# Optimization experiments

Hardware: AMD Instinct MI355X
Metric: run time of the kernel (lower is better)

The kernel has to match this reference:

```python
import jax, jax.numpy as jnp
import numpy as np

N_ENTITIES = 100000
N_EDGES = 500000
N_RELATIONS = 200
DIM = 64
HEADS = 4
POW_ITER = 5
ALPHA = 0.1
LEAKY_SLOPE = 0.01
EPS = 1e-16


def setup_inputs() -> dict:
    key = jax.random.key(0)
    ks = jax.random.split(key, 11)
    scale = 0.1
    return {
        "entity_embed": jax.random.normal(ks[0], (N_ENTITIES, DIM), jnp.float32),
        "relation_embed": jax.random.normal(ks[1], (N_RELATIONS, DIM), jnp.float32),
        "W_h": jax.random.normal(ks[2], (DIM, HEADS * DIM), jnp.float32) * scale,
        "W_t": jax.random.normal(ks[3], (DIM, HEADS * DIM), jnp.float32) * scale,
        "W_r": jax.random.normal(ks[4], (DIM, HEADS * DIM), jnp.float32) * scale,
        "att_h": jax.random.normal(ks[5], (HEADS, DIM), jnp.float32) * scale,
        "att_t": jax.random.normal(ks[6], (HEADS, DIM), jnp.float32) * scale,
        "att_r": jax.random.normal(ks[7], (HEADS, DIM), jnp.float32) * scale,
        "W_o": jax.random.normal(ks[8], (HEADS * DIM, DIM), jnp.float32) * scale,
        "edge_index": jax.random.randint(ks[9], (2, N_EDGES), 0, N_ENTITIES, jnp.int64),
        "edge_type": jax.random.randint(ks[10], (N_EDGES,), 0, N_RELATIONS, jnp.int64),
    }


def _segment_softmax(scores, seg_ids, num_segments):
    # scores: [E, heads]; softmax over edges sharing the same seg_id, per head
    m = jax.ops.segment_max(scores, seg_ids, num_segments=num_segments)
    e = jnp.exp(scores - m[seg_ids])
    denom = jax.ops.segment_sum(e, seg_ids, num_segments=num_segments)
    return e / (denom[seg_ids] + EPS)


def reference(entity_embed, relation_embed, W_h, W_t, W_r,
              att_h, att_t, att_r, W_o, edge_index, edge_type):
    head_ids, tail_ids = edge_index[0], edge_index[1]

    # per-edge gathered embeddings, projected per head: [E, heads, dim]
    Wh = (entity_embed[head_ids] @ W_h).reshape(-1, HEADS, DIM)
    Wt = (entity_embed[tail_ids] @ W_t).reshape(-1, HEADS, DIM)
    Wr = (relation_embed[edge_type] @ W_r).reshape(-1, HEADS, DIM)

    s_h = jnp.sum(jnp.tanh(Wh) * att_h[None], axis=-1)  # [E, heads]
    s_t = jnp.sum(jnp.tanh(Wt) * att_t[None], axis=-1)
    s_r = jnp.sum(jnp.tanh(Wr) * att_r[None], axis=-1)
    scores = jax.nn.leaky_relu(s_h + s_t + s_r, negative_slope=LEAKY_SLOPE)

    att = _segment_softmax(scores, head_ids, N_ENTITIES)  # [E, heads]
    A = (1.0 - ALPHA) * att

    # PPR power iteration, vectorized over heads: Z: [N, heads, dim]
    Z0 = entity_embed[:, None, :]  # [N, 1, dim]
    Z_init = jnp.broadcast_to(Z0, (N_ENTITIES, HEADS, DIM))

    def step(Z, _):
        msgs = A[:, :, None] * Z[tail_ids]  # [E, heads, dim]
        Z_new = jax.ops.segment_sum(msgs, head_ids, num_segments=N_ENTITIES) + ALPHA * Z0
        return Z_new, None

    Z, _ = jax.lax.scan(step, Z_init, None, length=POW_ITER)

    out = Z.reshape(N_ENTITIES, HEADS * DIM) @ W_o  # [N, dim]
    return out
```

## Files before the change

kernel.cpp:

```cpp
#include <hip/hip_runtime.h>
#include <hip/hip_fp16.h>
#include <math.h>

#define N_ENT 100000
#define N_EDGE 500000
#define N_REL 200

typedef short bf16x8 __attribute__((ext_vector_type(8)));
typedef float f32x4 __attribute__((ext_vector_type(4)));

__device__ __forceinline__ float fast_tanh(float x) {
    float xc = fminf(x, 15.f);
    float e = __expf(2.f * xc);
    return (e - 1.f) / (e + 1.f);
}

__device__ __forceinline__ unsigned short f2bf(float f) {
    unsigned u = __float_as_uint(f);
    unsigned r = u + 0x7FFF + ((u >> 16) & 1);
    return (unsigned short)(r >> 16);
}

__device__ __forceinline__ uint2 pack_half4(const float4 v) {
    __half2 lo = __floats2half2_rn(v.x, v.y);
    __half2 hi = __floats2half2_rn(v.z, v.w);
    uint2 r;
    r.x = *reinterpret_cast<const unsigned int*>(&lo);
    r.y = *reinterpret_cast<const unsigned int*>(&hi);
    return r;
}

__device__ __forceinline__ float4 unpack_half4(uint2 u) {
    __half2 lo = *reinterpret_cast<const __half2*>(&u.x);
    __half2 hi = *reinterpret_cast<const __half2*>(&u.y);
    float2 a = __half22float2(lo);
    float2 b = __half22float2(hi);
    return make_float4(a.x, a.y, b.x, b.y);
}

__global__ __launch_bounds__(256) void cvt_emb_kernel(
    const float* __restrict__ in, unsigned short* __restrict__ out, int nquads)
{
    for (int i = blockIdx.x * 256 + threadIdx.x; i < nquads; i += gridDim.x * 256) {
        float4 v = ((const float4*)in)[i];
        ushort4 o;
        o.x = f2bf(v.x); o.y = f2bf(v.y); o.z = f2bf(v.z); o.w = f2bf(v.w);
        ((ushort4*)out)[i] = o;
    }
}

__global__ __launch_bounds__(256) void cvt_wT_kernel(
    const float* __restrict__ W0, const float* __restrict__ W1,
    unsigned short* __restrict__ wT)
{
    int idx = blockIdx.x * 256 + threadIdx.x;
    if (idx >= 2 * 256 * 64) return;
    int mat = idx >> 14;
    int rem = idx & 16383;
    int col = rem >> 6;
    int k   = rem & 63;
    const float* W = (mat == 0) ? W0 : W1;
    wT[idx] = f2bf(W[k * 256 + col]);
}

__global__ __launch_bounds__(256) void proj_mfma_kernel(
    const unsigned short* __restrict__ emb_bf,
    const unsigned short* __restrict__ wT,
    const float* __restrict__ att0, const float* __restrict__ att1,
    float* __restrict__ p0, float* __restrict__ p1, int nrows)
{
    const int wv   = threadIdx.x >> 6;
    const int lane = threadIdx.x & 63;
    const int r4   = lane >> 4;
    const int cl   = lane & 15;
    const int rowbase = blockIdx.x * 64 + wv * 16;

    int ra = min(rowbase + cl, nrows - 1);
    bf16x8 a0 = *(const bf16x8*)(emb_bf + (size_t)ra * 64 + 8 * r4);
    bf16x8 a1 = *(const bf16x8*)(emb_bf + (size_t)ra * 64 + 8 * r4 + 32);

#pragma unroll
    for (int mat = 0; mat < 2; ++mat) {
        const float* att = (mat == 0) ? att0 : att1;
        float* p         = (mat == 0) ? p0 : p1;
        float pacc[4][4];
#pragma unroll
        for (int head = 0; head < 4; ++head) {
            float ph_[4] = {0.f, 0.f, 0.f, 0.f};
#pragma unroll
            for (int sub = 0; sub < 4; ++sub) {
                int col = head * 64 + sub * 16 + cl;
                const unsigned short* wp =
                    wT + ((size_t)(mat * 256 + col)) * 64 + 8 * r4;
                bf16x8 b0 = *(const bf16x8*)(wp);
                bf16x8 b1 = *(const bf16x8*)(wp + 32);
                f32x4 c = {0.f, 0.f, 0.f, 0.f};
                c = __builtin_amdgcn_mfma_f32_16x16x32_bf16(a0, b0, c, 0, 0, 0);
                c = __builtin_amdgcn_mfma_f32_16x16x32_bf16(a1, b1, c, 0, 0, 0);
                float av = att[head * 64 + sub * 16 + cl];
#pragma unroll
                for (int j = 0; j < 4; ++j) {
                    float v = fast_tanh(c[j]) * av;
                    v += __shfl_xor(v, 1, 64);
                    v += __shfl_xor(v, 2, 64);
                    v += __shfl_xor(v, 4, 64);
                    v += __shfl_xor(v, 8, 64);
                    ph_[j] += v;
                }
            }
#pragma unroll
            for (int j = 0; j < 4; ++j) pacc[head][j] = ph_[j];
        }
        if (cl == 0) {
#pragma unroll
            for (int j = 0; j < 4; ++j) {
                int row = rowbase + r4 * 4 + j;
                if (row < nrows) {
                    *(float4*)(p + (size_t)row * 4) = make_float4(
                        pacc[0][j], pacc[1][j], pacc[2][j], pacc[3][j]);
                }
            }
        }
    }
}

__global__ __launch_bounds__(256) void proj_gemm_kernel(
    const float* __restrict__ emb,
    const float* __restrict__ W0,
    const float* __restrict__ att0,
    float* __restrict__ p0,
    int nrows)
{
    __shared__ float e_lds[64][68];
    __shared__ float w0_lds[64][64];
    __shared__ float red[4][4][64];

    const int t    = threadIdx.x;
    const int wv   = t >> 6;
    const int lane = t & 63;
    const int er   = t & 15;
    const int d0   = (t >> 4) * 4;
    const int base = blockIdx.x * 64;

#pragma unroll
    for (int i = 0; i < 4; ++i) {
        int f = t + 256 * i;
        int row = f >> 4, c4 = f & 15;
        int gr = min(base + row, nrows - 1);
        float4 v = *(const float4*)(emb + (size_t)gr * 64 + 4 * c4);
        *(float4*)&e_lds[row][4 * c4] = v;
    }

    float p0s[4][4];

    for (int head = 0; head < 4; ++head) {
        {
            int k0 = t >> 4, c4 = t & 15;
#pragma unroll
            for (int kk = 0; kk < 4; ++kk) {
                int k = k0 + 16 * kk;
                *(float4*)&w0_lds[k][4 * c4] =
                    *(const float4*)(W0 + (size_t)k * 256 + head * 64 + 4 * c4);
            }
        }
        __syncthreads();

        float acc0[4][4] = {};
        for (int k4 = 0; k4 < 16; ++k4) {
            float4 z0 = *(const float4*)&e_lds[er +  0][4 * k4];
            float4 z1 = *(const float4*)&e_lds[er + 16][4 * k4];
            float4 z2 = *(const float4*)&e_lds[er + 32][4 * k4];
            float4 z3 = *(const float4*)&e_lds[er + 48][4 * k4];
            const float zr[4][4] = {
                {z0.x, z0.y, z0.z, z0.w},
                {z1.x, z1.y, z1.z, z1.w},
                {z2.x, z2.y, z2.z, z2.w},
                {z3.x, z3.y, z3.z, z3.w}};
#pragma unroll
            for (int jj = 0; jj < 4; ++jj) {
                float4 w0v = *(const float4*)&w0_lds[4 * k4 + jj][d0];
#pragma unroll
                for (int i = 0; i < 4; ++i) {
                    float zj = zr[i][jj];
                    acc0[i][0] = fmaf(zj, w0v.x, acc0[i][0]);
                    acc0[i][1] = fmaf(zj, w0v.y, acc0[i][1]);
                    acc0[i][2] = fmaf(zj, w0v.z, acc0[i][2]);
                    acc0[i][3] = fmaf(zj, w0v.w, acc0[i][3]);
                }
            }
        }

        float4 av0 = *(const float4*)(att0 + head * 64 + d0);
#pragma unroll
        for (int i = 0; i < 4; ++i) {
            float v = fast_tanh(acc0[i][0]) * av0.x
                    + fast_tanh(acc0[i][1]) * av0.y
                    + fast_tanh(acc0[i][2]) * av0.z
                    + fast_tanh(acc0[i][3]) * av0.w;
            v += __shfl_xor(v, 16, 64);
            v += __shfl_xor(v, 32, 64);
            p0s[head][i] = v;
        }
        __syncthreads();
    }

    if (lane < 16) {
#pragma unroll
        for (int h = 0; h < 4; ++h)
#pragma unroll
            for (int i = 0; i < 4; ++i)
                red[wv][h][lane + 16 * i] = p0s[h][i];
    }
    __syncthreads();
    if (t < 64) {
        int row = base + t;
        if (row < nrows) {
            float4 pv;
            pv.x = red[0][0][t] + red[1][0][t] + red[2][0][t] + red[3][0][t];
            pv.y = red[0][1][t] + red[1][1][t] + red[2][1][t] + red[3][1][t];
            pv.z = red[0][2][t] + red[1][2][t] + red[2][2][t] + red[3][2][t];
            pv.w = red[0][3][t] + red[1][3][t] + red[2][3][t] + red[3][3][t];
            *(float4*)(p0 + (size_t)row * 4) = pv;
        }
    }
}

__global__ __launch_bounds__(256) void hist_kernel(
    const int* __restrict__ eidx, int* __restrict__ counts)
{
    int e = blockIdx.x * 256 + threadIdx.x;
    if (e >= N_EDGE) return;
    atomicAdd(&counts[eidx[e]], 1);
}

__global__ __launch_bounds__(1024) void scan_kernel(
    const int* __restrict__ counts, int* __restrict__ row_start)
{
    __shared__ int wsum[16];
    __shared__ int carry_s;
    const int lane = threadIdx.x & 63;
    const int wid  = threadIdx.x >> 6;
    if (threadIdx.x == 0) carry_s = 0;
    __syncthreads();
    for (int base = 0; base < N_ENT; base += 4096) {
        int i0 = base + (int)threadIdx.x * 4;
        int4 v = make_int4(0, 0, 0, 0);
        if (i0 + 3 < N_ENT) v = *(const int4*)(counts + i0);
        else {
            if (i0 + 0 < N_ENT) v.x = counts[i0 + 0];
            if (i0 + 1 < N_ENT) v.y = counts[i0 + 1];
            if (i0 + 2 < N_ENT) v.z = counts[i0 + 2];
            if (i0 + 3 < N_ENT) v.w = counts[i0 + 3];
        }
        int s1 = v.x + v.y, s2 = s1 + v.z, tsum = s2 + v.w;
        int incl = tsum;
#pragma unroll
        for (int off = 1; off < 64; off <<= 1) {
            int t = __shfl_up(incl, off, 64);
            if (lane >= off) incl += t;
        }
        if (lane == 63) wsum[wid] = incl;
        __syncthreads();
        int wave_off = 0;
#pragma unroll
        for (int w = 0; w < 16; ++w)
            wave_off += (w < wid) ? wsum[w] : 0;
        int carry = carry_s;
        int excl = carry + wave_off + (incl - tsum);
        if (i0 + 3 < N_ENT) {
            *(int4*)(row_start + i0) = make_int4(excl, excl + v.x, excl + s1, excl + s2);
        } else {
            if (i0 + 0 < N_ENT) row_start[i0 + 0] = excl;
            if (i0 + 1 < N_ENT) row_start[i0 + 1] = excl + v.x;
            if (i0 + 2 < N_ENT) row_start[i0 + 2] = excl + s1;
            if (i0 + 3 < N_ENT) row_start[i0 + 3] = excl + s2;
        }
        __syncthreads();
        if (threadIdx.x == 1023) carry_s = carry + wave_off + incl;
    }
    __syncthreads();
    if (threadIdx.x == 0) row_start[N_ENT] = carry_s;
}

__global__ __launch_bounds__(256) void scatter_score_kernel(
    const int* __restrict__ eidx, const int* __restrict__ etype,
    const float* __restrict__ ph, const float* __restrict__ pt,
    const float* __restrict__ pr,
    const int* __restrict__ row_start, int* __restrict__ cursor,
    int* __restrict__ csr_col, float* __restrict__ csr_a)
{
    int e = blockIdx.x * 256 + threadIdx.x;
    if (e >= N_EDGE) return;
    int hn = eidx[e];
    int tn = eidx[N_EDGE + e];
    int r  = etype[e];
    float4 a = *(const float4*)(ph + (size_t)hn * 4);
    float4 b = *(const float4*)(pt + (size_t)tn * 4);
    float4 c = *(const float4*)(pr + (size_t)r * 4);
    float s0 = a.x + b.x + c.x;
    float s1 = a.y + b.y + c.y;
    float s2 = a.z + b.z + c.z;
    float s3 = a.w + b.w + c.w;
    s0 = s0 >= 0.f ? s0 : 0.01f * s0;
    s1 = s1 >= 0.f ? s1 : 0.01f * s1;
    s2 = s2 >= 0.f ? s2 : 0.01f * s2;
    s3 = s3 >= 0.f ? s3 : 0.01f * s3;
    float4 ev = make_float4(__expf(s0), __expf(s1), __expf(s2), __expf(s3));
    int pos = row_start[hn] + atomicAdd(&cursor[hn], 1);
    csr_col[pos] = tn;
    *(float4*)(csr_a + (size_t)pos * 4) = ev;
}

__global__ __launch_bounds__(256) void normalize_kernel(
    const int* __restrict__ row_start, float* __restrict__ csr_a)
{
    const int wid  = threadIdx.x >> 6;
    const int lane = threadIdx.x & 63;
    const int n = blockIdx.x * 4 + wid;
    if (n >= N_ENT) return;
    const int s   = row_start[n];
    const int end = row_start[n + 1];
    const int nf  = (end - s) * 4;

    float sum = 0.f;
    for (int f = lane; f < nf; f += 64)
        sum += csr_a[(size_t)s * 4 + f];
#pragma unroll
    for (int off = 4; off < 64; off <<= 1)
        sum += __shfl_xor(sum, off, 64);
    float scale = 0.9f / (sum + 1e-16f);
    for (int f = lane; f < nf; f += 64)
        csr_a[(size_t)s * 4 + f] *= scale;
}

template <bool IN_HALF, bool OUT_HALF>
__global__ __launch_bounds__(256) void spmm_kernel(
    const void* __restrict__ Zin_v, const float* __restrict__ emb,
    const int* __restrict__ row_start, const int* __restrict__ csr_col,
    const float* __restrict__ csr_a, void* __restrict__ Zout_v)
{
    const int wave = threadIdx.x >> 6;
    const int lane = threadIdx.x & 63;
    const int n = blockIdx.x * 4 + wave;
    const int h = lane >> 4;
    const __half* Zin_h = (const __half*)Zin_v;

    const float4* e4 = (const float4*)emb;
    float4 zi = e4[(size_t)n * 16 + (lane & 15)];
    float4 acc0 = make_float4(0.1f * zi.x, 0.1f * zi.y, 0.1f * zi.z, 0.1f * zi.w);
    float4 acc1 = make_float4(0.f, 0.f, 0.f, 0.f);
    float4 acc2 = make_float4(0.f, 0.f, 0.f, 0.f);
    float4 acc3 = make_float4(0.f, 0.f, 0.f, 0.f);

    const int s   = row_start[n];
    const int end = row_start[n + 1];

    auto zrow = [&](int c) -> float4 {
        if (IN_HALF) {
            uint2 u = *(const uint2*)(Zin_h + (size_t)c * 256 + 4 * lane);
            return unpack_half4(u);
        } else {
            return *(const float4*)(emb + (size_t)c * 64 + 4 * (lane & 15));
        }
    };
    auto fma4 = [](float4& acc, float a, const float4& z) {
        acc.x = fmaf(a, z.x, acc.x);
        acc.y = fmaf(a, z.y, acc.y);
        acc.z = fmaf(a, z.z, acc.z);
        acc.w = fmaf(a, z.w, acc.w);
    };

    for (int b = s; b < end; b += 16) {
        const int nb = min(16, end - b);
        int   cl = (lane < nb) ? csr_col[b + lane] : 0;
        float al = (lane < nb * 4) ? csr_a[(size_t)b * 4 + lane] : 0.f;

        int j = 0;
        for (; j + 4 <= nb; j += 4) {
            int c0 = __shfl(cl, j + 0, 64);
            int c1 = __shfl(cl, j + 1, 64);
            int c2 = __shfl(cl, j + 2, 64);
            int c3 = __shfl(cl, j + 3, 64);
            float a0 = __shfl(al, (j + 0) * 4 + h, 64);
            float a1 = __shfl(al, (j + 1) * 4 + h, 64);
            float a2 = __shfl(al, (j + 2) * 4 + h, 64);
            float a3 = __shfl(al, (j + 3) * 4 + h, 64);
            float4 za = zrow(c0);
            float4 zb = zrow(c1);
            float4 zc = zrow(c2);
            float4 zd = zrow(c3);
            fma4(acc0, a0, za);
            fma4(acc1, a1, zb);
            fma4(acc2, a2, zc);
            fma4(acc3, a3, zd);
        }
        if (j + 0 < nb) {
            int c = __shfl(cl, j + 0, 64);
            float a = __shfl(al, (j + 0) * 4 + h, 64);
            float4 z = zrow(c);
            fma4(acc0, a, z);
        }
        if (j + 1 < nb) {
            int c = __shfl(cl, j + 1, 64);
            float a = __shfl(al, (j + 1) * 4 + h, 64);
            float4 z = zrow(c);
            fma4(acc1, a, z);
        }
        if (j + 2 < nb) {
            int c = __shfl(cl, j + 2, 64);
            float a = __shfl(al, (j + 2) * 4 + h, 64);
            float4 z = zrow(c);
            fma4(acc2, a, z);
        }
    }
    acc0.x += acc1.x + acc2.x + acc3.x;
    acc0.y += acc1.y + acc2.y + acc3.y;
    acc0.z += acc1.z + acc2.z + acc3.z;
    acc0.w += acc1.w + acc2.w + acc3.w;

    if (OUT_HALF)
        *(uint2*)((__half*)Zout_v + (size_t)n * 256 + 4 * lane) = pack_half4(acc0);
    else
        *(float4*)((float*)Zout_v + (size_t)n * 256 + 4 * lane) = acc0;
}

__global__ __launch_bounds__(256) void outproj_kernel(
    const float* __restrict__ Z, const float* __restrict__ Wo,
    float* __restrict__ out)
{
    __shared__ float z_lds[64][68];
    __shared__ float w_lds[64][64];
    const int t = threadIdx.x;
    const int base = blockIdx.x * 64;
    const int er = t & 15;
    const int d0 = (t >> 4) * 4;

    float acc[4][4] = {};
    for (int kc = 0; kc < 4; ++kc) {
        {
            const float4* src = (const float4*)(Wo + (size_t)kc * 64 * 64);
            float4* dst = (float4*)&w_lds[0][0];
#pragma unroll
            for (int i = 0; i < 4; ++i)
                dst[t + 256 * i] = src[t + 256 * i];
        }
        {
#pragma unroll
            for (int i = 0; i < 4; ++i) {
                int f = t + 256 * i;
                int row = f >> 4, c4 = f & 15;
                int gr = min(base + row, N_ENT - 1);
                float4 v = *(const float4*)(Z + (size_t)gr * 256 + kc * 64 + 4 * c4);
                *(float4*)&z_lds[row][4 * c4] = v;
            }
        }
        __syncthreads();

        for (int k4 = 0; k4 < 16; ++k4) {
            float4 z0 = *(const float4*)&z_lds[er +  0][4 * k4];
            float4 z1 = *(const float4*)&z_lds[er + 16][4 * k4];
            float4 z2 = *(const float4*)&z_lds[er + 32][4 * k4];
            float4 z3 = *(const float4*)&z_lds[er + 48][4 * k4];
#pragma unroll
            for (int jj = 0; jj < 4; ++jj) {
                float4 wv = *(const float4*)&w_lds[4 * k4 + jj][d0];
                float zj0 = ((const float*)&z0)[jj];
                float zj1 = ((const float*)&z1)[jj];
                float zj2 = ((const float*)&z2)[jj];
                float zj3 = ((const float*)&z3)[jj];
                acc[0][0] = fmaf(zj0, wv.x, acc[0][0]);
                acc[0][1] = fmaf(zj0, wv.y, acc[0][1]);
                acc[0][2] = fmaf(zj0, wv.z, acc[0][2]);
                acc[0][3] = fmaf(zj0, wv.w, acc[0][3]);
                acc[1][0] = fmaf(zj1, wv.x, acc[1][0]);
                acc[1][1] = fmaf(zj1, wv.y, acc[1][1]);
                acc[1][2] = fmaf(zj1, wv.z, acc[1][2]);
                acc[1][3] = fmaf(zj1, wv.w, acc[1][3]);
                acc[2][0] = fmaf(zj2, wv.x, acc[2][0]);
                acc[2][1] = fmaf(zj2, wv.y, acc[2][1]);
                acc[2][2] = fmaf(zj2, wv.z, acc[2][2]);
                acc[2][3] = fmaf(zj2, wv.w, acc[2][3]);
                acc[3][0] = fmaf(zj3, wv.x, acc[3][0]);
                acc[3][1] = fmaf(zj3, wv.y, acc[3][1]);
                acc[3][2] = fmaf(zj3, wv.z, acc[3][2]);
                acc[3][3] = fmaf(zj3, wv.w, acc[3][3]);
            }
        }
        __syncthreads();
    }

#pragma unroll
    for (int i = 0; i < 4; ++i) {
        int row = base + er + 16 * i;
        if (row < N_ENT) {
            *(float4*)(out + (size_t)row * 64 + d0) =
                make_float4(acc[i][0], acc[i][1], acc[i][2], acc[i][3]);
        }
    }
}

extern "C" void kernel_launch(void* const* d_in, const int* in_sizes, int n_in,
                              void* d_out, int out_size, void* d_ws, size_t ws_size,
                              hipStream_t stream)
{
    const float* entity = (const float*)d_in[0];
    const float* rel    = (const float*)d_in[1];
    const float* W_h    = (const float*)d_in[2];
    const float* W_t    = (const float*)d_in[3];
    const float* W_r    = (const float*)d_in[4];
    const float* att_h  = (const float*)d_in[5];
    const float* att_t  = (const float*)d_in[6];
    const float* att_r  = (const float*)d_in[7];
    const float* W_o    = (const float*)d_in[8];
    const int*   eidx   = (const int*)d_in[9];
    const int*   etype  = (const int*)d_in[10];
    float* out = (float*)d_out;

    char* ws = (char*)d_ws;
    size_t off = 0;
    auto alloc = [&](size_t bytes) -> void* {
        void* p = ws + off;
        off += (bytes + 255) & ~(size_t)255;
        return p;
    };
    float* p_h      = (float*)alloc((size_t)N_ENT * 4 * 4);
    float* p_t      = (float*)alloc((size_t)N_ENT * 4 * 4);
    float* p_r      = (float*)alloc((size_t)N_REL * 4 * 4);
    int*   counts   = (int*)alloc((size_t)N_ENT * 4);
    int*   row_start= (int*)alloc(((size_t)N_ENT + 1) * 4);
    int*   cursor   = (int*)alloc((size_t)N_ENT * 4);
    int*   csr_col  = (int*)alloc((size_t)N_EDGE * 4);
    float* csr_a    = (float*)alloc((size_t)N_EDGE * 4 * 4);
    float* Zf       = (float*)alloc((size_t)N_ENT * 256 * 4);
    __half* Zh_b    = (__half*)Zf;
    __half* Zh_a    = (__half*)alloc((size_t)N_ENT * 256 * 2);
    unsigned short* emb_bf = (unsigned short*)alloc((size_t)N_ENT * 64 * 2);
    unsigned short* wT     = (unsigned short*)alloc((size_t)2 * 256 * 64 * 2);

    hipMemsetAsync(counts, 0, (size_t)N_ENT * 4, stream);
    hipMemsetAsync(cursor, 0, (size_t)N_ENT * 4, stream);

    cvt_emb_kernel<<<2048, 256, 0, stream>>>(entity, emb_bf, N_ENT * 64 / 4);
    cvt_wT_kernel<<<(2 * 256 * 64 + 255) / 256, 256, 0, stream>>>(W_h, W_t, wT);

    proj_mfma_kernel<<<(N_ENT + 63) / 64, 256, 0, stream>>>(
        emb_bf, wT, att_h, att_t, p_h, p_t, N_ENT);
    proj_gemm_kernel<<<(N_REL + 63) / 64, 256, 0, stream>>>(
        rel, W_r, att_r, p_r, N_REL);

    hist_kernel<<<(N_EDGE + 255) / 256, 256, 0, stream>>>(eidx, counts);
    scan_kernel<<<1, 1024, 0, stream>>>(counts, row_start);
    scatter_score_kernel<<<(N_EDGE + 255) / 256, 256, 0, stream>>>(
        eidx, etype, p_h, p_t, p_r, row_start, cursor, csr_col, csr_a);
    normalize_kernel<<<(N_ENT + 3) / 4, 256, 0, stream>>>(row_start, csr_a);

    spmm_kernel<false, true ><<<N_ENT / 4, 256, 0, stream>>>(nullptr, entity, row_start, csr_col, csr_a, Zh_b);
    spmm_kernel<true,  true ><<<N_ENT / 4, 256, 0, stream>>>(Zh_b, entity, row_start, csr_col, csr_a, Zh_a);
    spmm_kernel<true,  true ><<<N_ENT / 4, 256, 0, stream>>>(Zh_a, entity, row_start, csr_col, csr_a, Zh_b);
    spmm_kernel<true,  true ><<<N_ENT / 4, 256, 0, stream>>>(Zh_b, entity, row_start, csr_col, csr_a, Zh_a);
    spmm_kernel<true,  false><<<N_ENT / 4, 256, 0, stream>>>(Zh_a, entity, row_start, csr_col, csr_a, Zf);

    outproj_kernel<<<(N_ENT + 63) / 64, 256, 0, stream>>>(Zf, W_o, out);
}
```

Before: 497.8 us.

## Use fp16 MFMA for output projection and keep final Z in half

The last power-iteration step now writes Z in fp16 instead of fp32. The output projection is replaced by an MFMA kernel that reads the fp16 Z directly and uses a transposed fp16 copy of W_o made by a new conversion kernel. This halves Z traffic on the final write and read, and moves the scalar-FMA LDS GEMM onto matrix cores. The projection kernel also defers its cross-lane shuffle reduction until after the sub-tile accumulation, cutting shuffles. The cost is extra rounding of the final Z and of W_o to fp16, plus one small extra launch.

```diff
diff --git a/kernel.cpp b/kernel.cpp
--- a/kernel.cpp
+++ b/kernel.cpp
@@ -7,6 +7,7 @@
 #define N_REL 200
 
 typedef short bf16x8 __attribute__((ext_vector_type(8)));
+typedef _Float16 f16x8 __attribute__((ext_vector_type(8)));
 typedef float f32x4 __attribute__((ext_vector_type(4)));
 
 __device__ __forceinline__ float fast_tanh(float x) {
@@ -63,6 +64,16 @@
     wT[idx] = f2bf(W[k * 256 + col]);
 }
 
+__global__ __launch_bounds__(256) void cvt_woT_kernel(
+    const float* __restrict__ Wo, __half* __restrict__ woT)
+{
+    int idx = blockIdx.x * 256 + threadIdx.x;
+    if (idx >= 64 * 256) return;
+    int d = idx >> 8;
+    int k = idx & 255;
+    woT[idx] = __float2half(Wo[k * 64 + d]);
+}
+
 __global__ __launch_bounds__(256) void proj_mfma_kernel(
     const unsigned short* __restrict__ emb_bf,
     const unsigned short* __restrict__ wT,
@@ -86,7 +97,7 @@
         float pacc[4][4];
 #pragma unroll
         for (int head = 0; head < 4; ++head) {
-            float ph_[4] = {0.f, 0.f, 0.f, 0.f};
+            float vsum[4] = {0.f, 0.f, 0.f, 0.f};
 #pragma unroll
             for (int sub = 0; sub < 4; ++sub) {
                 int col = head * 64 + sub * 16 + cl;
@@ -99,17 +110,18 @@
                 c = __builtin_amdgcn_mfma_f32_16x16x32_bf16(a1, b1, c, 0, 0, 0);
                 float av = att[head * 64 + sub * 16 + cl];
 #pragma unroll
-                for (int j = 0; j < 4; ++j) {
-                    float v = fast_tanh(c[j]) * av;
-                    v += __shfl_xor(v, 1, 64);
-                    v += __shfl_xor(v, 2, 64);
-                    v += __shfl_xor(v, 4, 64);
-                    v += __shfl_xor(v, 8, 64);
-                    ph_[j] += v;
-                }
+                for (int j = 0; j < 4; ++j)
+                    vsum[j] = fmaf(fast_tanh(c[j]), av, vsum[j]);
             }
 #pragma unroll
-            for (int j = 0; j < 4; ++j) pacc[head][j] = ph_[j];
+            for (int j = 0; j < 4; ++j) {
+                float v = vsum[j];
+                v += __shfl_xor(v, 1, 64);
+                v += __shfl_xor(v, 2, 64);
+                v += __shfl_xor(v, 4, 64);
+                v += __shfl_xor(v, 8, 64);
+                pacc[head][j] = v;
+            }
         }
         if (cl == 0) {
 #pragma unroll
@@ -424,77 +436,39 @@
         *(float4*)((float*)Zout_v + (size_t)n * 256 + 4 * lane) = acc0;
 }
 
-__global__ __launch_bounds__(256) void outproj_kernel(
-    const float* __restrict__ Z, const float* __restrict__ Wo,
+__global__ __launch_bounds__(256) void outproj_mfma_kernel(
+    const __half* __restrict__ Z,
+    const __half* __restrict__ woT,
     float* __restrict__ out)
 {
-    __shared__ float z_lds[64][68];
-    __shared__ float w_lds[64][64];
-    const int t = threadIdx.x;
-    const int base = blockIdx.x * 64;
-    const int er = t & 15;
-    const int d0 = (t >> 4) * 4;
-
-    float acc[4][4] = {};
-    for (int kc = 0; kc < 4; ++kc) {
-        {
-            const float4* src = (const float4*)(Wo + (size_t)kc * 64 * 64);
-            float4* dst = (float4*)&w_lds[0][0];
-#pragma unroll
-            for (int i = 0; i < 4; ++i)
-                dst[t + 256 * i] = src[t + 256 * i];
-        }
-        {
-#pragma unroll
-            for (int i = 0; i < 4; ++i) {
-                int f = t + 256 * i;
-                int row = f >> 4, c4 = f & 15;
-                int gr = min(base + row, N_ENT - 1);
-                float4 v = *(const float4*)(Z + (size_t)gr * 256 + kc * 64 + 4 * c4);
-                *(float4*)&z_lds[row][4 * c4] = v;
-            }
-        }
-        __syncthreads();
-
-        for (int k4 = 0; k4 < 16; ++k4) {
-            float4 z0 = *(const float4*)&z_lds[er +  0][4 * k4];
-            float4 z1 = *(const float4*)&z_lds[er + 16][4 * k4];
-            float4 z2 = *(const float4*)&z_lds[er + 32][4 * k4];
-            float4 z3 = *(const float4*)&z_lds[er + 48][4 * k4];
-#pragma unroll
-            for (int jj = 0; jj < 4; ++jj) {
-                float4 wv = *(const float4*)&w_lds[4 * k4 + jj][d0];
-                float zj0 = ((const float*)&z0)[jj];
-                float zj1 = ((const float*)&z1)[jj];
-                float zj2 = ((const float*)&z2)[jj];
-                float zj3 = ((const float*)&z3)[jj];
-                acc[0][0] = fmaf(zj0, wv.x, acc[0][0]);
-                acc[0][1] = fmaf(zj0, wv.y, acc[0][1]);
-                acc[0][2] = fmaf(zj0, wv.z, acc[0][2]);
-                acc[0][3] = fmaf(zj0, wv.w, acc[0][3]);
-                acc[1][0] = fmaf(zj1, wv.x, acc[1][0]);
-                acc[1][1] = fmaf(zj1, wv.y, acc[1][1]);
-                acc[1][2] = fmaf(zj1, wv.z, acc[1][2]);
-                acc[1][3] = fmaf(zj1, wv.w, acc[1][3]);
-                acc[2][0] = fmaf(zj2, wv.x, acc[2][0]);
-                acc[2][1] = fmaf(zj2, wv.y, acc[2][1]);
-                acc[2][2] = fmaf(zj2, wv.z, acc[2][2]);
-                acc[2][3] = fmaf(zj2, wv.w, acc[2][3]);
-                acc[3][0] = fmaf(zj3, wv.x, acc[3][0]);
-                acc[3][1] = fmaf(zj3, wv.y, acc[3][1]);
-                acc[3][2] = fmaf(zj3, wv.z, acc[3][2]);
-                acc[3][3] = fmaf(zj3, wv.w, acc[3][3]);
-            }
-        }
-        __syncthreads();
-    }
-
-#pragma unroll
-    for (int i = 0; i < 4; ++i) {
-        int row = base + er + 16 * i;
-        if (row < N_ENT) {
-            *(float4*)(out + (size_t)row * 64 + d0) =
-                make_float4(acc[i][0], acc[i][1], acc[i][2], acc[i][3]);
+    const int wv   = threadIdx.x >> 6;
+    const int lane = threadIdx.x & 63;
+    const int cl   = lane & 15;
+    const int r4   = lane >> 4;
+    const int rowbase = blockIdx.x * 64 + wv * 16;
+
+    int ra = min(rowbase + cl, N_ENT - 1);
+    const _Float16* zp = (const _Float16*)(Z + (size_t)ra * 256);
+    f16x8 a[8];
+#pragma unroll
+    for (int ks = 0; ks < 8; ++ks)
+        a[ks] = *(const f16x8*)(zp + ks * 32 + 8 * r4);
+
+    const _Float16* wp = (const _Float16*)woT;
+#pragma unroll
+    for (int st = 0; st < 4; ++st) {
+        f32x4 c = {0.f, 0.f, 0.f, 0.f};
+        const _Float16* wcol = wp + (size_t)(st * 16 + cl) * 256 + 8 * r4;
+#pragma unroll
+        for (int ks = 0; ks < 8; ++ks) {
+            f16x8 b = *(const f16x8*)(wcol + ks * 32);
+            c = __builtin_amdgcn_mfma_f32_16x16x32_f16(a[ks], b, c, 0, 0, 0);
+        }
+#pragma unroll
+        for (int j = 0; j < 4; ++j) {
+            int row = rowbase + r4 * 4 + j;
+            if (row < N_ENT)
+                out[(size_t)row * 64 + st * 16 + cl] = c[j];
         }
     }
 }
@@ -531,17 +505,18 @@
     int*   cursor   = (int*)alloc((size_t)N_ENT * 4);
     int*   csr_col  = (int*)alloc((size_t)N_EDGE * 4);
     float* csr_a    = (float*)alloc((size_t)N_EDGE * 4 * 4);
-    float* Zf       = (float*)alloc((size_t)N_ENT * 256 * 4);
-    __half* Zh_b    = (__half*)Zf;
     __half* Zh_a    = (__half*)alloc((size_t)N_ENT * 256 * 2);
+    __half* Zh_b    = (__half*)alloc((size_t)N_ENT * 256 * 2);
     unsigned short* emb_bf = (unsigned short*)alloc((size_t)N_ENT * 64 * 2);
     unsigned short* wT     = (unsigned short*)alloc((size_t)2 * 256 * 64 * 2);
+    __half* woT     = (__half*)alloc((size_t)64 * 256 * 2);
 
     hipMemsetAsync(counts, 0, (size_t)N_ENT * 4, stream);
     hipMemsetAsync(cursor, 0, (size_t)N_ENT * 4, stream);
 
     cvt_emb_kernel<<<2048, 256, 0, stream>>>(entity, emb_bf, N_ENT * 64 / 4);
     cvt_wT_kernel<<<(2 * 256 * 64 + 255) / 256, 256, 0, stream>>>(W_h, W_t, wT);
+    cvt_woT_kernel<<<(64 * 256 + 255) / 256, 256, 0, stream>>>(W_o, woT);
 
     proj_mfma_kernel<<<(N_ENT + 63) / 64, 256, 0, stream>>>(
         emb_bf, wT, att_h, att_t, p_h, p_t, N_ENT);
@@ -558,7 +533,7 @@
     spmm_kernel<true,  true ><<<N_ENT / 4, 256, 0, stream>>>(Zh_b, entity, row_start, csr_col, csr_a, Zh_a);
     spmm_kernel<true,  true ><<<N_ENT / 4, 256, 0, stream>>>(Zh_a, entity, row_start, csr_col, csr_a, Zh_b);
     spmm_kernel<true,  true ><<<N_ENT / 4, 256, 0, stream>>>(Zh_b, entity, row_start, csr_col, csr_a, Zh_a);
-    spmm_kernel<true,  false><<<N_ENT / 4, 256, 0, stream>>>(Zh_a, entity, row_start, csr_col, csr_a, Zf);
-
-    outproj_kernel<<<(N_ENT + 63) / 64, 256, 0, stream>>>(Zf, W_o, out);
-}
+    spmm_kernel<true,  true ><<<N_ENT / 4, 256, 0, stream>>>(Zh_a, entity, row_start, csr_col, csr_a, Zh_b);
+
+    outproj_mfma_kernel<<<(N_ENT + 63) / 64, 256, 0, stream>>>(Zh_b, woT, out);
+}
```

Result: faster. 460.8 us (-7.4%).
